# Kernel optimization log

Measured on AMD Instinct MI355X. Metric: run time of the kernel, lower is better.

The kernel has to match this reference:

```python
import jax, jax.numpy as jnp
import numpy as np
from jax.scipy.special import logsumexp

B, L, M, D = 8192, 1024, 128, 2  # batch, hilbert.size, bond dim, local_size
MACHINE_POW = 2


def setup_inputs() -> dict:
    key = jax.random.key(0)
    k1, k2 = jax.random.split(key)
    # configurations in the zero-magnetization sector: each row is a permutation
    # of L//2 zeros and L//2 ones (constrained HomogeneousHilbert)
    base = jnp.tile(jnp.arange(D, dtype=jnp.int32), L // D)  # (L,)
    inputs = jax.vmap(lambda k: jax.random.permutation(k, base))(jax.random.split(k1, B))
    # variational parameters epsilon: (local_size, M, size); centered at 1 so the
    # length-L multiplicative cache chain stays in fp32 range
    epsilon = 1.0 + 0.02 * jax.random.normal(k2, (D, M, L), dtype=jnp.float32)
    return {"inputs": inputs, "epsilon": epsilon}


def _conditionals(inputs, epsilon):
    # inputs: (B, L) int in [0, D); epsilon: (D, M, L)
    Bn, Ln = inputs.shape
    Dn, Mn, _ = epsilon.shape
    half = Ln // 2

    def scan_fun(carry, index):
        cache, n_spins = carry                       # (B, D, M), (B, D)
        prev = inputs[:, (index - 1) % Ln]           # (B,) previous-site state
        params_i = epsilon[:, :, index]              # (D, M)
        # irregular gather: cache[b, prev[b], :]
        gathered = jnp.take_along_axis(cache, prev[:, None, None], axis=1)[:, 0, :]  # (B, M)
        prods = params_i[None, :, :] * gathered[:, None, :]  # (B, D, M)
        log_psi = jnp.sum(prods, axis=-1)            # (B, D) sum over bond dim
        n_spins = jnp.where(index > 0,
                            n_spins + jax.nn.one_hot(prev, Dn, dtype=jnp.int32),
                            n_spins)
        # zero-magnetization renormalization: -inf once a local state is exhausted
        renorm = jnp.log(jnp.heaviside((half - n_spins).astype(log_psi.dtype), 0.0))
        return (prods, n_spins), log_psi + renorm

    cache0 = jnp.ones((Bn, Dn, Mn), epsilon.dtype)
    n0 = jnp.zeros((Bn, Dn), jnp.int32)
    _, log_psi = jax.lax.scan(scan_fun, (cache0, n0), jnp.arange(Ln))
    return jnp.transpose(log_psi, (1, 0, 2))  # (B, L, D)


def reference(inputs, epsilon):
    lp = _conditionals(inputs, epsilon)  # (B, L, D)
    # normalize conditionals over local states (machine_pow = 2)
    lp = lp - (1.0 / MACHINE_POW) * logsumexp(MACHINE_POW * lp, axis=-1, keepdims=True)
    # pick the log-conditional of the actual configuration at each site
    sel = jnp.take_along_axis(lp, inputs[:, :, None], axis=2)[:, :, 0]  # (B, L)
    # n_symm = 1 (default apply_symmetries): symmetrized logsumexp is identity
    return jnp.sum(sel, axis=1)  # (B,) log_psi
```

## Files before the change

### kernel.cpp

```cpp
#include <hip/hip_runtime.h>
#include <hip/hip_fp16.h>

typedef unsigned long long u64;
typedef unsigned int uint32;
typedef short short8 __attribute__((ext_vector_type(8)));
typedef float f32x4 __attribute__((ext_vector_type(4)));
typedef _Float16 h2 __attribute__((ext_vector_type(2)));

#define B_N 8192
#define L_N 1024
#define M_N 128
#define HALF_N 512

#define OFF_WE   0x0
#define OFF_CW   0x20000
#define OFF_LR   0x120000
#define OFF_BITS 0x160000
#define OFF_T    0x260000
#define OFF_RQ   0x280000

#define PACK_BLK 2048
#define PACK_IT  16
#define EPS_BLK  32
#define ZERO_BLK 32

__device__ __forceinline__ unsigned short f32_bf16(float f) {
    union { float f; unsigned u; } x; x.f = f;
    unsigned u = x.u + 0x7FFFu + ((x.u >> 16) & 1u);
    return (unsigned short)(u >> 16);
}

__device__ __forceinline__ float fdot2(h2 a, h2 b, float c) {
#if __has_builtin(__builtin_amdgcn_fdot2)
    return __builtin_amdgcn_fdot2(a, b, c, false);
#else
    return (float)a[0] * (float)b[0] + (float)a[1] * (float)b[1] + c;
#endif
}

__device__ __forceinline__ uint32 fas_u(float f) { union { float f; uint32 u; } x; x.f = f; return x.u; }
__device__ __forceinline__ float uas_f(uint32 u) { union { uint32 u; float f; } x; x.u = u; return x.f; }

__device__ __forceinline__ float exp2_n(float x) {
#if __has_builtin(__builtin_amdgcn_exp2f)
    return __builtin_amdgcn_exp2f(x);
#else
    return exp2f(x);
#endif
}
__device__ __forceinline__ float log2_n(float x) {
#if __has_builtin(__builtin_amdgcn_logf)
    return __builtin_amdgcn_logf(x);
#else
    return __log2f(x);
#endif
}
__device__ __forceinline__ uint32 bfe1(uint32 v, int off) {
#if __has_builtin(__builtin_amdgcn_sbfe)
    return (uint32)__builtin_amdgcn_sbfe((int)v, off, 1);
#else
    return (uint32)((int)(v << (31 - off)) >> 31);
#endif
}
__device__ __forceinline__ uint32 ubfe2(uint32 v, int off) {
#if __has_builtin(__builtin_amdgcn_ubfe)
    return (uint32)__builtin_amdgcn_ubfe((int)v, off, 2);
#else
    return (v >> off) & 3u;
#endif
}

template<int CTRL>
__device__ __forceinline__ float dpp_add(float x, float y) {
    union { float f; int i; } a, r;
    a.f = y;
    r.i = __builtin_amdgcn_update_dpp(0, a.i, CTRL, 0xF, 0xF, true);
    return x + r.f;
}

union HU { uint32 u; __half2 hh; h2 v2; };

__global__ __launch_bounds__(256) void k_prep(const int* __restrict__ inp,
        const float* __restrict__ eps, u64* __restrict__ bits,
        _Float16* __restrict__ wE, _Float16* __restrict__ cw,
        unsigned short* __restrict__ lrT, float* __restrict__ out) {
    int bid = blockIdx.x;
    if (bid < PACK_BLK) {
        int g = bid * 256 + threadIdx.x;
        const int stride = PACK_BLK * 256;
        #pragma unroll 4
        for (int it = 0; it < PACK_IT; ++it) {
            int v = inp[g];
            u64 m = __ballot(v != 0);
            if ((threadIdx.x & 63) == 0) bits[g >> 6] = m;
            g += stride;
        }
        return;
    }
    bid -= PACK_BLK;
    if (bid < EPS_BLK) {
        int wid = threadIdx.x >> 6, lane = threadIdx.x & 63;
        int m = bid * 4 + wid;
        const float* e0 = eps + (size_t)m * L_N + lane * 16;
        const float* e1 = eps + (size_t)(M_N + m) * L_N + lane * 16;
        float a[16], b[16];
        #pragma unroll
        for (int j = 0; j < 16; j += 4) {
            *(float4*)&a[j] = *(const float4*)&e0[j];
            *(float4*)&b[j] = *(const float4*)&e1[j];
        }
        float local = 1.f;
        #pragma unroll
        for (int j = 0; j < 16; ++j) local *= a[j];
        float sc = local;
        #pragma unroll
        for (int d = 1; d < 64; d <<= 1) {
            float up = __shfl_up(sc, d);
            if (lane >= d) sc *= up;
        }
        float prev = __shfl_up(sc, 1);
        float E = (lane == 0) ? 1.f : prev;
        int i0 = lane * 16;
        float rat_e = 1.f, w_e = 0.f;
        #pragma unroll
        for (int j = 0; j < 16; ++j) {
            float rat = b[j] / a[j];
            float w = E * (a[j] - b[j]);
            lrT[(size_t)m * L_N + i0 + j] = f32_bf16(__log2f(rat));
            int u = (i0 + j) >> 1;
            if ((j & 1) == 0) {
                wE[(size_t)u * M_N + m] = (_Float16)w;
                rat_e = rat;
            } else {
                _Float16* cr = cw + (size_t)u * 4 * 256;
                float wo1 = w * rat_e;
                cr[0 * 256 + m]       = (_Float16)0.f;
                cr[0 * 256 + 128 + m] = (_Float16)w;
                cr[1 * 256 + m]       = (_Float16)(rat_e - 1.f);
                cr[1 * 256 + 128 + m] = (_Float16)wo1;
                cr[2 * 256 + m]       = (_Float16)(rat - 1.f);
                cr[2 * 256 + 128 + m] = (_Float16)w;
                cr[3 * 256 + m]       = (_Float16)(rat_e * rat - 1.f);
                cr[3 * 256 + 128 + m] = (_Float16)wo1;
            }
            E *= a[j];
        }
        (void)w_e;
        return;
    }
    bid -= EPS_BLK;
    if (bid < ZERO_BLK) {
        out[bid * 256 + threadIdx.x] = 0.f;
    }
}

template<int CN>
__global__ __launch_bounds__(256) void k_slog2(const u64* __restrict__ bits,
        const unsigned short* __restrict__ lrT, _Float16* __restrict__ Rq,
        int* __restrict__ T) {
    if (blockIdx.x >= 1024) {
        int b = (blockIdx.x - 1024) * 256 + threadIdx.x;
        const u64* brow = bits + (size_t)b * 16;
        int n1 = 0, n0 = 0, Tv = 1024;
        for (int wd = 0; wd < 16; ++wd) {
            u64 x = brow[wd];
            int pc = __popcll(x);
            if (n1 + pc < HALF_N && n0 + (64 - pc) < HALF_N) {
                n1 += pc; n0 += 64 - pc;
                continue;
            }
            int found = 0;
            for (int k = 0; k < 64; ++k) {
                if (n1 >= HALF_N || n0 >= HALF_N) { Tv = wd * 64 + k; found = 1; break; }
                int sb = (int)((x >> k) & 1);
                n1 += sb; n0 += 1 - sb;
            }
            if (!found) Tv = (wd + 1) * 64;
            break;
        }
        T[b] = Tv;
        return;
    }
    int btile = blockIdx.x >> 1;
    int half = blockIdx.x & 1;
    int wid = threadIdx.x >> 6, lane = threadIdx.x & 63;
    int col = lane & 15, quad = lane >> 4;
    int m = (half * 4 + wid) * 16 + col;
    int b_row = btile * 16 + col;
    const u64* brow = bits + (size_t)b_row * 16;
    const unsigned short* lrow = lrT + (size_t)m * L_N;

    f32x4 cum = (f32x4){0.f, 0.f, 0.f, 0.f};

    for (int w = 0; w < 16; ++w) {
        u64 wv = brow[w];
        #pragma unroll
        for (int hf = 0; hf < 2; ++hf) {
            if (CN == 32 || hf == 0) {
                int cc = (CN == 32) ? (w * 2 + hf) : w;
                #pragma unroll
                for (int reg = 0; reg < 4; ++reg) {
                    int b = btile * 16 + quad * 4 + reg;
                    Rq[((size_t)cc * B_N + b) * M_N + m] = (_Float16)exp2_n(cum[reg]);
                }
            }
            short8 a;
            #pragma unroll
            for (int j = 0; j < 8; ++j)
                a[j] = (short)((((wv >> (hf * 32 + quad * 8 + j)) & 1) != 0) ? 0x3F80 : 0);
            union { uint4 u; short8 s; } bf;
            bf.u = *(const uint4*)(lrow + w * 64 + hf * 32 + quad * 8);
            cum = __builtin_amdgcn_mfma_f32_16x16x32_bf16(a, bf.s, cum, 0, 0, 0);
        }
    }
}

template<int CN>
__global__ __launch_bounds__(256) __attribute__((amdgpu_waves_per_eu(1, 4)))
void k_main(const u64* __restrict__ bits, const _Float16* __restrict__ wE,
        const _Float16* __restrict__ cw, const _Float16* __restrict__ Rq,
        const int* __restrict__ T, float* __restrict__ out) {
    constexpr int CHN = L_N / CN;
    constexpr int CSH = (CN == 16) ? 4 : 5;
    __shared__ _Float16 webuf[16 * M_N];
    __shared__ _Float16 cwbuf[16 * 4 * 256];
    int c = blockIdx.x & (CN - 1);
    int bblk = blockIdx.x >> CSH;
    int lane = threadIdx.x & 63, wid = threadIdx.x >> 6;
    int s = lane & 7, grp = lane >> 3;
    int q = s & 3;
    int b0 = bblk * 128 + wid * 32 + grp * 4;

    HU R2[4][8];
    u64 wb[4];
    const int word0 = (c * CHN) >> 6;
    const int hs0 = ((c * CHN) >> 5) & 1;
    #pragma unroll
    for (int k = 0; k < 4; ++k) {
        int b = b0 + (q ^ k);
        union { uint4 v[2]; uint32 w[8]; } P;
        const uint4* src = (const uint4*)(Rq + ((size_t)c * B_N + b) * M_N + s * 16);
        P.v[0] = src[0]; P.v[1] = src[1];
        #pragma unroll
        for (int j = 0; j < 8; ++j) R2[k][j].u = P.w[j];
        wb[k] = bits[(size_t)b * 16 + word0];
    }
    int Tb = T[b0 + q];

    const float LOG2E2 = 2.885390082f;
    const float NHL2 = -0.3465735903f;
    float sum = 0.f;
    #pragma unroll
    for (int h = 0; h < CHN / 32; ++h) {
        if (h) __syncthreads();
        {
            size_t pbase = (size_t)c * (CHN / 2) + h * 16;
            const uint4* se = (const uint4*)(wE + pbase * M_N);
            const uint4* sc = (const uint4*)(cw + pbase * 4 * 256);
            ((uint4*)webuf)[threadIdx.x] = se[threadIdx.x];
            #pragma unroll
            for (int t = 0; t < 8; ++t)
                ((uint4*)cwbuf)[threadIdx.x + t * 256] = sc[threadIdx.x + t * 256];
        }
        __syncthreads();

        int sh = ((hs0 + h) & 1) * 32;
        uint32 wh[4];
        #pragma unroll
        for (int k = 0; k < 4; ++k) wh[k] = (uint32)(wb[k] >> sh);
        uint32 ows = ~wh[0];
        int rel = Tb - (c * CHN + h * 32);
        uint32 vmask = (rel <= 0) ? 0u : ((rel >= 32) ? 0xFFFFFFFFu : ((1u << rel) - 1u));

        #pragma unroll 2
        for (int tt = 0; tt < 16; ++tt) {
            union U8 { uint4 q4[2]; uint32 w[8]; h2 v2[8]; __half2 hh[8]; };
            U8 WEu;
            const _Float16* web = &webuf[tt * M_N + s * 16];
            WEu.q4[0] = *(const uint4*)web;
            WEu.q4[1] = *((const uint4*)web + 1);

            int pb = tt * 1024 + s * 16;
            int ad[4];
            #pragma unroll
            for (int k = 0; k < 4; ++k)
                ad[k] = pb + (int)(ubfe2(wh[k], 2 * tt) << 8);

            float de[4];
            #pragma unroll
            for (int k = 0; k < 4; ++k) {
                float acc = 0.f;
                #pragma unroll
                for (int j = 0; j < 8; ++j) acc = fdot2(R2[k][j].v2, WEu.v2[j], acc);
                de[k] = acc;
            }
            float dd[4];
            #pragma unroll
            for (int k = 0; k < 4; ++k) {
                U8 WOu;
                WOu.q4[0] = *(const uint4*)&cwbuf[ad[k] + 128];
                WOu.q4[1] = *((const uint4*)&cwbuf[ad[k] + 128] + 1);
                float acc = 0.f;
                #pragma unroll
                for (int j = 0; j < 8; ++j) acc = fdot2(R2[k][j].v2, WOu.v2[j], acc);
                dd[k] = acc;
            }
            float xe = dpp_add<0xB1>(de[0], de[1]);
            float ye = dpp_add<0xB1>(de[2], de[3]);
            float De = dpp_add<0x4E>(xe, ye);
            De = dpp_add<0x104>(De, De);
            float xo = dpp_add<0xB1>(dd[0], dd[1]);
            float yo = dpp_add<0xB1>(dd[2], dd[3]);
            float Do = dpp_add<0x4E>(xo, yo);
            Do = dpp_add<0x104>(Do, Do);

            uint32 sg0 = bfe1(ows, 2 * tt) & 0x80000000u;
            float l0 = log2_n(1.f + exp2_n(LOG2E2 * uas_f(fas_u(De) ^ sg0)));
            sum = fmaf(NHL2, uas_f(fas_u(l0) & bfe1(vmask, 2 * tt)), sum);
            uint32 sg1 = bfe1(ows, 2 * tt + 1) & 0x80000000u;
            float l1 = log2_n(1.f + exp2_n(LOG2E2 * uas_f(fas_u(Do) ^ sg1)));
            sum = fmaf(NHL2, uas_f(fas_u(l1) & bfe1(vmask, 2 * tt + 1)), sum);

            #pragma unroll
            for (int k = 0; k < 4; ++k) {
                U8 CMu;
                CMu.q4[0] = *(const uint4*)&cwbuf[ad[k]];
                CMu.q4[1] = *((const uint4*)&cwbuf[ad[k]] + 1);
                #pragma unroll
                for (int j = 0; j < 8; ++j)
                    R2[k][j].hh = __hfma2(CMu.hh[j], R2[k][j].hh, R2[k][j].hh);
            }
        }
    }
    if (s < 4) atomicAdd(&out[b0 + s], sum);
}

extern "C" void kernel_launch(void* const* d_in, const int* in_sizes, int n_in,
                              void* d_out, int out_size, void* d_ws, size_t ws_size,
                              hipStream_t stream) {
    const int*   inputs  = (const int*)d_in[0];
    const float* epsilon = (const float*)d_in[1];
    float* out = (float*)d_out;

    char* ws = (char*)d_ws;
    _Float16* wE  = (_Float16*)(ws + OFF_WE);
    _Float16* cw  = (_Float16*)(ws + OFF_CW);
    unsigned short* lrT = (unsigned short*)(ws + OFF_LR);
    u64*   bits   = (u64*)  (ws + OFF_BITS);
    int*   T      = (int*)  (ws + OFF_T);
    _Float16* Rq  = (_Float16*)(ws + OFF_RQ);

    k_prep<<<PACK_BLK + EPS_BLK + ZERO_BLK, 256, 0, stream>>>(
        inputs, epsilon, bits, wE, cw, lrT, out);

    const size_t need32 = (size_t)OFF_RQ + (size_t)32 * B_N * M_N * 2;
    if (ws_size >= need32) {
        k_slog2<32><<<1024 + 32, 256, 0, stream>>>(bits, lrT, Rq, T);
        k_main<32><<<(B_N / 128) * 32, 256, 0, stream>>>(bits, wE, cw, Rq, T, out);
    } else {
        k_slog2<16><<<1024 + 32, 256, 0, stream>>>(bits, lrT, Rq, T);
        k_main<16><<<(B_N / 128) * 16, 256, 0, stream>>>(bits, wE, cw, Rq, T, out);
    }
}
```

Baseline: 162.5 us.

## Split odd-site weights into uniform dot products and swizzle multiplier table in LDS

Replaces the per-sample gathered odd-site weight vector with three uniform weight rows (even, odd, and a correction term selected by the previous bit). All lanes now read the same shared-memory weights instead of divergent addresses, at the cost of one extra dot product per sample per step. The multiplier table is shrunk to 512 halves per pair and stored XOR-swizzled to reduce LDS bank conflicts on the data-dependent gather. LDS footprint and global staging traffic also shrink.

```diff
diff --git a/kernel.cpp b/kernel.cpp
--- a/kernel.cpp
+++ b/kernel.cpp
@@ -12,12 +12,12 @@
 #define M_N 128
 #define HALF_N 512
 
-#define OFF_WE   0x0
-#define OFF_CW   0x20000
-#define OFF_LR   0x120000
-#define OFF_BITS 0x160000
-#define OFF_T    0x260000
-#define OFF_RQ   0x280000
+#define OFF_WS   0x0
+#define OFF_CMB  0x60000
+#define OFF_LR   0xE0000
+#define OFF_BITS 0x120000
+#define OFF_T    0x220000
+#define OFF_RQ   0x240000
 
 #define PACK_BLK 2048
 #define PACK_IT  16
@@ -82,7 +82,7 @@
 
 __global__ __launch_bounds__(256) void k_prep(const int* __restrict__ inp,
         const float* __restrict__ eps, u64* __restrict__ bits,
-        _Float16* __restrict__ wE, _Float16* __restrict__ cw,
+        _Float16* __restrict__ wS, _Float16* __restrict__ cmb,
         unsigned short* __restrict__ lrT, float* __restrict__ out) {
     int bid = blockIdx.x;
     if (bid < PACK_BLK) {
@@ -129,23 +129,20 @@
             lrT[(size_t)m * L_N + i0 + j] = f32_bf16(__log2f(rat));
             int u = (i0 + j) >> 1;
             if ((j & 1) == 0) {
-                wE[(size_t)u * M_N + m] = (_Float16)w;
-                rat_e = rat;
+                rat_e = rat; w_e = w;
             } else {
-                _Float16* cr = cw + (size_t)u * 4 * 256;
-                float wo1 = w * rat_e;
-                cr[0 * 256 + m]       = (_Float16)0.f;
-                cr[0 * 256 + 128 + m] = (_Float16)w;
-                cr[1 * 256 + m]       = (_Float16)(rat_e - 1.f);
-                cr[1 * 256 + 128 + m] = (_Float16)wo1;
-                cr[2 * 256 + m]       = (_Float16)(rat - 1.f);
-                cr[2 * 256 + 128 + m] = (_Float16)w;
-                cr[3 * 256 + m]       = (_Float16)(rat_e * rat - 1.f);
-                cr[3 * 256 + 128 + m] = (_Float16)wo1;
+                _Float16* wr = wS + (size_t)u * 384;
+                wr[m]       = (_Float16)w_e;
+                wr[128 + m] = (_Float16)w;
+                wr[256 + m] = (_Float16)(w * (rat_e - 1.f));
+                _Float16* cr = cmb + (size_t)u * 512;
+                cr[m]       = (_Float16)0.f;
+                cr[128 + m] = (_Float16)(rat_e - 1.f);
+                cr[256 + m] = (_Float16)(rat - 1.f);
+                cr[384 + m] = (_Float16)(rat_e * rat - 1.f);
             }
             E *= a[j];
         }
-        (void)w_e;
         return;
     }
     bid -= EPS_BLK;
@@ -217,13 +214,13 @@
 
 template<int CN>
 __global__ __launch_bounds__(256) __attribute__((amdgpu_waves_per_eu(1, 4)))
-void k_main(const u64* __restrict__ bits, const _Float16* __restrict__ wE,
-        const _Float16* __restrict__ cw, const _Float16* __restrict__ Rq,
+void k_main(const u64* __restrict__ bits, const _Float16* __restrict__ wS,
+        const _Float16* __restrict__ cmb, const _Float16* __restrict__ Rq,
         const int* __restrict__ T, float* __restrict__ out) {
     constexpr int CHN = L_N / CN;
     constexpr int CSH = (CN == 16) ? 4 : 5;
-    __shared__ _Float16 webuf[16 * M_N];
-    __shared__ _Float16 cwbuf[16 * 4 * 256];
+    __shared__ _Float16 wsbuf[16 * 384];
+    __shared__ _Float16 cbuf [16 * 512];
     int c = blockIdx.x & (CN - 1);
     int bblk = blockIdx.x >> CSH;
     int lane = threadIdx.x & 63, wid = threadIdx.x >> 6;
@@ -255,12 +252,16 @@
         if (h) __syncthreads();
         {
             size_t pbase = (size_t)c * (CHN / 2) + h * 16;
-            const uint4* se = (const uint4*)(wE + pbase * M_N);
-            const uint4* sc = (const uint4*)(cw + pbase * 4 * 256);
-            ((uint4*)webuf)[threadIdx.x] = se[threadIdx.x];
-            #pragma unroll
-            for (int t = 0; t < 8; ++t)
-                ((uint4*)cwbuf)[threadIdx.x + t * 256] = sc[threadIdx.x + t * 256];
+            const uint4* ss = (const uint4*)(wS + pbase * 384);
+            const uint4* sc = (const uint4*)(cmb + pbase * 512);
+            #pragma unroll
+            for (int t = 0; t < 3; ++t)
+                ((uint4*)wsbuf)[threadIdx.x + t * 256] = ss[threadIdx.x + t * 256];
+            #pragma unroll
+            for (int t = 0; t < 4; ++t) {
+                int idx = threadIdx.x + t * 256;
+                ((uint4*)cbuf)[idx ^ (((idx >> 4) & 3) << 1)] = sc[idx];
+            }
         }
         __syncthreads();
 
@@ -275,44 +276,45 @@
         #pragma unroll 2
         for (int tt = 0; tt < 16; ++tt) {
             union U8 { uint4 q4[2]; uint32 w[8]; h2 v2[8]; __half2 hh[8]; };
-            U8 WEu;
-            const _Float16* web = &webuf[tt * M_N + s * 16];
-            WEu.q4[0] = *(const uint4*)web;
-            WEu.q4[1] = *((const uint4*)web + 1);
-
-            int pb = tt * 1024 + s * 16;
-            int ad[4];
-            #pragma unroll
-            for (int k = 0; k < 4; ++k)
-                ad[k] = pb + (int)(ubfe2(wh[k], 2 * tt) << 8);
-
-            float de[4];
+            int bs = tt * 384 + s * 16;
+            U8 WEu, WOu, WDu;
+            WEu.q4[0] = *(const uint4*)&wsbuf[bs];
+            WEu.q4[1] = *((const uint4*)&wsbuf[bs] + 1);
+            WOu.q4[0] = *(const uint4*)&wsbuf[bs + 128];
+            WOu.q4[1] = *((const uint4*)&wsbuf[bs + 128] + 1);
+            WDu.q4[0] = *(const uint4*)&wsbuf[bs + 256];
+            WDu.q4[1] = *((const uint4*)&wsbuf[bs + 256] + 1);
+
+            int cbo[4];
+            #pragma unroll
+            for (int k = 0; k < 4; ++k) cbo[k] = (int)ubfe2(wh[k], 2 * tt);
+
+            float de[4], dq[4], dd[4];
             #pragma unroll
             for (int k = 0; k < 4; ++k) {
-                float acc = 0.f;
+                float ae = 0.f, ao = 0.f, ad2 = 0.f;
                 #pragma unroll
-                for (int j = 0; j < 8; ++j) acc = fdot2(R2[k][j].v2, WEu.v2[j], acc);
-                de[k] = acc;
-            }
-            float dd[4];
-            #pragma unroll
-            for (int k = 0; k < 4; ++k) {
-                U8 WOu;
-                WOu.q4[0] = *(const uint4*)&cwbuf[ad[k] + 128];
-                WOu.q4[1] = *((const uint4*)&cwbuf[ad[k] + 128] + 1);
-                float acc = 0.f;
-                #pragma unroll
-                for (int j = 0; j < 8; ++j) acc = fdot2(R2[k][j].v2, WOu.v2[j], acc);
-                dd[k] = acc;
+                for (int j = 0; j < 8; ++j) {
+                    ae = fdot2(R2[k][j].v2, WEu.v2[j], ae);
+                    ao = fdot2(R2[k][j].v2, WOu.v2[j], ao);
+                    ad2 = fdot2(R2[k][j].v2, WDu.v2[j], ad2);
+                }
+                de[k] = ae; dq[k] = ao; dd[k] = ad2;
             }
             float xe = dpp_add<0xB1>(de[0], de[1]);
             float ye = dpp_add<0xB1>(de[2], de[3]);
             float De = dpp_add<0x4E>(xe, ye);
             De = dpp_add<0x104>(De, De);
-            float xo = dpp_add<0xB1>(dd[0], dd[1]);
-            float yo = dpp_add<0xB1>(dd[2], dd[3]);
-            float Do = dpp_add<0x4E>(xo, yo);
-            Do = dpp_add<0x104>(Do, Do);
+            float xq = dpp_add<0xB1>(dq[0], dq[1]);
+            float yq = dpp_add<0xB1>(dq[2], dq[3]);
+            float Dq = dpp_add<0x4E>(xq, yq);
+            Dq = dpp_add<0x104>(Dq, Dq);
+            float xd = dpp_add<0xB1>(dd[0], dd[1]);
+            float yd = dpp_add<0xB1>(dd[2], dd[3]);
+            float Dd = dpp_add<0x4E>(xd, yd);
+            Dd = dpp_add<0x104>(Dd, Dd);
+
+            float Do = Dq + uas_f(fas_u(Dd) & bfe1(wh[0], 2 * tt));
 
             uint32 sg0 = bfe1(ows, 2 * tt) & 0x80000000u;
             float l0 = log2_n(1.f + exp2_n(LOG2E2 * uas_f(fas_u(De) ^ sg0)));
@@ -324,8 +326,9 @@
             #pragma unroll
             for (int k = 0; k < 4; ++k) {
                 U8 CMu;
-                CMu.q4[0] = *(const uint4*)&cwbuf[ad[k]];
-                CMu.q4[1] = *((const uint4*)&cwbuf[ad[k]] + 1);
+                int ad = tt * 512 + (cbo[k] << 7) + ((s ^ cbo[k]) << 4);
+                CMu.q4[0] = *(const uint4*)&cbuf[ad];
+                CMu.q4[1] = *((const uint4*)&cbuf[ad] + 1);
                 #pragma unroll
                 for (int j = 0; j < 8; ++j)
                     R2[k][j].hh = __hfma2(CMu.hh[j], R2[k][j].hh, R2[k][j].hh);
@@ -343,22 +346,22 @@
     float* out = (float*)d_out;
 
     char* ws = (char*)d_ws;
-    _Float16* wE  = (_Float16*)(ws + OFF_WE);
-    _Float16* cw  = (_Float16*)(ws + OFF_CW);
+    _Float16* wS  = (_Float16*)(ws + OFF_WS);
+    _Float16* cmb = (_Float16*)(ws + OFF_CMB);
     unsigned short* lrT = (unsigned short*)(ws + OFF_LR);
     u64*   bits   = (u64*)  (ws + OFF_BITS);
     int*   T      = (int*)  (ws + OFF_T);
     _Float16* Rq  = (_Float16*)(ws + OFF_RQ);
 
     k_prep<<<PACK_BLK + EPS_BLK + ZERO_BLK, 256, 0, stream>>>(
-        inputs, epsilon, bits, wE, cw, lrT, out);
+        inputs, epsilon, bits, wS, cmb, lrT, out);
 
     const size_t need32 = (size_t)OFF_RQ + (size_t)32 * B_N * M_N * 2;
     if (ws_size >= need32) {
         k_slog2<32><<<1024 + 32, 256, 0, stream>>>(bits, lrT, Rq, T);
-        k_main<32><<<(B_N / 128) * 32, 256, 0, stream>>>(bits, wE, cw, Rq, T, out);
+        k_main<32><<<(B_N / 128) * 32, 256, 0, stream>>>(bits, wS, cmb, Rq, T, out);
     } else {
         k_slog2<16><<<1024 + 32, 256, 0, stream>>>(bits, lrT, Rq, T);
-        k_main<16><<<(B_N / 128) * 16, 256, 0, stream>>>(bits, wE, cw, Rq, T, out);
-    }
-}
+        k_main<16><<<(B_N / 128) * 16, 256, 0, stream>>>(bits, wS, cmb, Rq, T, out);
+    }
+}
```

Result: slower. 171.0 us (+5.2%).
